# Performance work log

Measured on AMD Instinct MI355X. Metric: run time of the kernel, lower is better.

The kernel has to match this reference:

```python
import jax, jax.numpy as jnp
import numpy as np

N_NODES = 100000
N_EDGES = 1600000
IN_FEATS = 256
N_HIDDEN = 128
N_CLASSES = 40


def setup_inputs() -> dict:
    key = jax.random.key(0)
    k1, k2, k3, k4, k5 = jax.random.split(key, 5)
    features = jax.random.normal(k1, (N_NODES, IN_FEATS), dtype=jnp.float32)
    edge_src = jax.random.randint(k2, (N_EDGES,), 0, N_NODES, dtype=jnp.int64)
    edge_dst = jax.random.randint(k3, (N_EDGES,), 0, N_NODES, dtype=jnp.int64)
    # GraphConv weights (Glorot-ish scaling)
    W1 = jax.random.normal(k4, (IN_FEATS, N_HIDDEN), dtype=jnp.float32) / np.sqrt(IN_FEATS)
    b1 = jnp.zeros((N_HIDDEN,), dtype=jnp.float32)
    W2 = jax.random.normal(k5, (N_HIDDEN, N_CLASSES), dtype=jnp.float32) / np.sqrt(N_HIDDEN)
    b2 = jnpspace = None
    b2 = jnp.zeros((N_CLASSES,), dtype=jnp.float32)
    return {"features": features, "edge_src": edge_src, "edge_dst": edge_dst,
            "W1": W1, "b1": b1, "W2": W2, "b2": b2}


def _degree_norms(edge_src, edge_dst, n_nodes):
    ones = jnp.ones(edge_src.shape[0], dtype=jnp.float32)
    deg_out = jax.ops.segment_sum(ones, edge_src, num_segments=n_nodes)
    deg_in = jax.ops.segment_sum(ones, edge_dst, num_segments=n_nodes)
    norm_src = jax.lax.rsqrt(jnp.clip(deg_out, 1.0))  # D_out^{-1/2}
    norm_dst = jax.lax.rsqrt(jnp.clip(deg_in, 1.0))   # D_in^{-1/2}
    return norm_src, norm_dst


def _graph_conv(x, W, b, edge_src, edge_dst, norm_src, norm_dst, activation=None):
    # DGL GraphConv norm='both': out = D_in^{-1/2} A D_out^{-1/2} (x W) + b
    h = (x @ W) * norm_src[:, None]                       # transform then src-normalize
    agg = jax.ops.segment_sum(h[edge_src], edge_dst,
                              num_segments=x.shape[0])    # sparse neighbor aggregation
    out = agg * norm_dst[:, None] + b
    if activation is not None:
        out = activation(out)
    return out


def reference(features, edge_src, edge_dst, W1, b1, W2, b2):
    norm_src, norm_dst = _degree_norms(edge_src, edge_dst, features.shape[0])
    h = _graph_conv(features, W1, b1, edge_src, edge_dst, norm_src, norm_dst,
                    activation=jax.nn.relu)
    # dropout is identity in eval-mode reference
    out = _graph_conv(h, W2, b2, edge_src, edge_dst, norm_src, norm_dst)
    return out
```

## Files before the change

kernel.cpp:

```cpp
#include <hip/hip_runtime.h>
#include <hip/hip_bf16.h>
#include <hip/hip_fp16.h>

#define NN 100000
#define NE 1600000
#define KF 256
#define NH 128
#define NC 40
#define PAD 64
#define CMAX 63

#define NBLK_P 512
#define PCHUNK (NE / NBLK_P)
#define BUK 256
#define NBUK ((NN + BUK - 1) / BUK)
#define CAP 6144

typedef __attribute__((ext_vector_type(8))) short bf16x8;
typedef __attribute__((ext_vector_type(4))) float f32x4;


__device__ __forceinline__ float ldf(const void* p, size_t i, bool bf){
  return bf ? __bfloat162float(((const __hip_bfloat16*)p)[i]) : ((const float*)p)[i];
}
__device__ __forceinline__ void cv2(unsigned int v, float* o){
  union { unsigned int i; float f; } a, b;
  a.i = v << 16; b.i = v & 0xffff0000u;
  o[0] = a.f; o[1] = b.f;
}
__device__ __forceinline__ void splitbf(float f, short* h, short* lo){
  union { float f; unsigned int u; } a; a.f = f;
  *h = (short)(a.u >> 16);
  union { unsigned int u; float f; } c; c.u = a.u & 0xffff0000u;
  union { float f; unsigned int u; } d; d.f = f - c.f;
  *lo = (short)(d.u >> 16);
}

__global__ void k_sniff_edges(const unsigned int* __restrict__ e, unsigned int* __restrict__ flags){
  __shared__ unsigned int sh[256];
  unsigned int v = 0;
  for (int i = blockIdx.x * 256 + threadIdx.x; i < NE / 2; i += gridDim.x * 256)
    v |= e[2 * i + 1];
  sh[threadIdx.x] = v;
  __syncthreads();
  for (int off = 128; off; off >>= 1){
    if (threadIdx.x < off) sh[threadIdx.x] |= sh[threadIdx.x + off];
    __syncthreads();
  }
  if (threadIdx.x == 0 && sh[0]) atomicOr(&flags[0], sh[0]);
}

__global__ void k_sniff_float(const unsigned int* __restrict__ w, unsigned int* __restrict__ flags){
  __shared__ unsigned int sh[256];
  unsigned int hits = 0;
  for (int i = blockIdx.x * 256 + threadIdx.x; i < (1 << 20); i += gridDim.x * 256){
    unsigned int b = (w[i] >> 7) & 0xFFu;
    hits += (b >= 118u && b <= 130u) ? 1u : 0u;
  }
  sh[threadIdx.x] = hits;
  __syncthreads();
  for (int off = 128; off; off >>= 1){
    if (threadIdx.x < off) sh[threadIdx.x] += sh[threadIdx.x + off];
    __syncthreads();
  }
  if (threadIdx.x == 0) atomicAdd(&flags[1], sh[0]);
}

__device__ __forceinline__ int edge_at(const void* p, int e, bool is64){
  return is64 ? (int)((const long long*)p)[e] : ((const int*)p)[e];
}
__device__ __forceinline__ bool f_isbf(const unsigned int* flags){ return flags[1] > (1u << 19); }

__global__ __launch_bounds__(256) void k_part(const void* __restrict__ src,
    const void* __restrict__ dst, const unsigned int* __restrict__ flags,
    int* __restrict__ deg_out, int* __restrict__ gcur, unsigned int* __restrict__ part){
  __shared__ int cnt[NBUK];
  __shared__ int base[NBUK];
  const bool is64 = (flags[0] == 0u);
  const int beg = blockIdx.x * PCHUNK;
  const int end = min(beg + PCHUNK, NE);
  for (int t = threadIdx.x; t < NBUK; t += 256) cnt[t] = 0;
  __syncthreads();
  for (int e = beg + threadIdx.x; e < end; e += 256){
    int d = edge_at(dst, e, is64);
    atomicAdd(&cnt[d >> 8], 1);
  }
  __syncthreads();
  for (int t = threadIdx.x; t < NBUK; t += 256){
    int c = cnt[t];
    base[t] = c ? atomicAdd(&gcur[t], c) : 0;
    cnt[t] = 0;
  }
  __syncthreads();
  for (int e = beg + threadIdx.x; e < end; e += 256){
    int d = edge_at(dst, e, is64);
    int s = edge_at(src, e, is64);
    atomicAdd(&deg_out[s], 1);
    int b = d >> 8;
    int pos = base[b] + atomicAdd(&cnt[b], 1);
    if (pos < CAP)
      part[(size_t)b * CAP + pos] = ((unsigned int)s << 8) | (unsigned int)(d & 255);
  }
}

__global__ __launch_bounds__(256) void k_csr(const unsigned int* __restrict__ part,
    const int* __restrict__ gcur, int* __restrict__ fill, int* __restrict__ csr_pad){
  __shared__ int rows[256 * CMAX];
  __shared__ int fl[256];
  const int b = blockIdx.x;
  fl[threadIdx.x] = 0;
  __syncthreads();
  const int n = min(gcur[b], CAP);
  for (int i = threadIdx.x; i < n; i += 256){
    unsigned int e = part[(size_t)b * CAP + i];
    int r = (int)(e & 255u);
    int s = (int)(e >> 8);
    int pos = atomicAdd(&fl[r], 1);
    if (pos < CMAX) rows[r * CMAX + pos] = s;
  }
  __syncthreads();
  const int node0 = b * BUK;
  if (node0 + threadIdx.x < NN) fill[node0 + threadIdx.x] = fl[threadIdx.x];
  for (int idx = threadIdx.x; idx < 256 * CMAX; idx += 256){
    int r = idx / CMAX;
    int c = idx - r * CMAX;
    int node = node0 + r;
    if (node < NN) csr_pad[node * PAD + c] = rows[idx];
  }
}

__global__ void k_norms(const int* __restrict__ deg_out, const int* __restrict__ fill,
                        float* __restrict__ nsrc, float* __restrict__ ndst){
  int i = blockIdx.x * 256 + threadIdx.x;
  if (i < NN){
    nsrc[i] = rsqrtf(fmaxf((float)deg_out[i], 1.f));
    ndst[i] = rsqrtf(fmaxf((float)fill[i], 1.f));
  }
}

__global__ void k_w1s(const void* __restrict__ W1, const unsigned int* __restrict__ flags,
                      bf16x8* __restrict__ w1s){
  if (!f_isbf(flags)) return;
  int idx = blockIdx.x * 256 + threadIdx.x;
  if (idx >= 4096) return;
  int l    = idx & 63;
  int tile = idx >> 6;
  int kt   = tile >> 3;
  int nt   = tile & 7;
  int krow = kt * 32 + (l >> 4) * 8;
  int col  = nt * 16 + (l & 15);
  const unsigned short* w = (const unsigned short*)W1;
  bf16x8 v;
  #pragma unroll
  for (int j = 0; j < 8; j++)
    v[j] = (short)w[(size_t)(krow + j) * NH + col];
  w1s[idx] = v;
}
__global__ void k_w1s_f32(const void* __restrict__ W1, const unsigned int* __restrict__ flags,
                          bf16x8* __restrict__ w1h, bf16x8* __restrict__ w1l){
  if (f_isbf(flags)) return;
  int idx = blockIdx.x * 256 + threadIdx.x;
  if (idx >= 4096) return;
  int l    = idx & 63;
  int tile = idx >> 6;
  int kt   = tile >> 3;
  int nt   = tile & 7;
  int krow = kt * 32 + (l >> 4) * 8;
  int col  = nt * 16 + (l & 15);
  const float* w = (const float*)W1;
  bf16x8 vh, vl;
  #pragma unroll
  for (int j = 0; j < 8; j++){
    short h, lo;
    splitbf(w[(size_t)(krow + j) * NH + col], &h, &lo);
    vh[j] = h; vl[j] = lo;
  }
  w1h[idx] = vh;
  w1l[idx] = vl;
}

__global__ __launch_bounds__(256) void k_gemm1_mfma(const void* __restrict__ feat,
    const bf16x8* __restrict__ w1s, const unsigned int* __restrict__ flags,
    const float* __restrict__ nsrc, __half* __restrict__ h1){
  if (!f_isbf(flags)) return;
  const int t  = threadIdx.x;
  const int wv = t >> 6;
  const int l  = t & 63;
  const int row0 = blockIdx.x * 64 + wv * 16;
  const int arow = row0 + (l & 15);
  const short* fp = (const short*)feat;
  const size_t abase = (size_t)min(arow, NN - 1) * KF + (l >> 4) * 8;

  f32x4 acc[8];
  #pragma unroll
  for (int n = 0; n < 8; n++) acc[n] = (f32x4){0.f, 0.f, 0.f, 0.f};

  #pragma unroll 2
  for (int kt = 0; kt < 8; kt++){
    bf16x8 a = *(const bf16x8*)(fp + abase + kt * 32);
    #pragma unroll
    for (int n = 0; n < 8; n++){
      bf16x8 b = w1s[(kt * 8 + n) * 64 + l];
      acc[n] = __builtin_amdgcn_mfma_f32_16x16x32_bf16(a, b, acc[n], 0, 0, 0);
    }
  }
  const int rbase = row0 + (l >> 4) * 4;
  const int col   = l & 15;
  #pragma unroll
  for (int i = 0; i < 4; i++){
    int r = rbase + i;
    if (r < NN){
      float s = nsrc[r];
      #pragma unroll
      for (int n = 0; n < 8; n++)
        h1[(size_t)r * NH + n * 16 + col] = __float2half_rn(acc[n][i] * s);
    }
  }
}

__global__ __launch_bounds__(256) void k_gemm1_mf32(const float* __restrict__ feat,
    const bf16x8* __restrict__ w1h, const bf16x8* __restrict__ w1l,
    const unsigned int* __restrict__ flags,
    const float* __restrict__ nsrc, __half* __restrict__ h1){
  if (f_isbf(flags)) return;
  const int t  = threadIdx.x;
  const int wv = t >> 6;
  const int l  = t & 63;
  const int row0 = blockIdx.x * 128 + wv * 32;
  const int ar0 = row0 + (l & 15);
  const int ar1 = ar0 + 16;
  const float* fp0 = feat + (size_t)min(ar0, NN - 1) * KF + (l >> 4) * 8;
  const float* fp1 = feat + (size_t)min(ar1, NN - 1) * KF + (l >> 4) * 8;

  f32x4 acc[2][8];
  #pragma unroll
  for (int g = 0; g < 2; g++)
    #pragma unroll
    for (int n = 0; n < 8; n++) acc[g][n] = (f32x4){0.f, 0.f, 0.f, 0.f};

  for (int kt = 0; kt < 8; kt++){
    float4 u0 = *(const float4*)(fp0 + kt * 32);
    float4 u1 = *(const float4*)(fp0 + kt * 32 + 4);
    float4 v0 = *(const float4*)(fp1 + kt * 32);
    float4 v1 = *(const float4*)(fp1 + kt * 32 + 4);
    bf16x8 a0h, a0l, a1h, a1l;
    {
      const float* uf = (const float*)&u0;
      const float* vf = (const float*)&v0;
      #pragma unroll
      for (int j = 0; j < 4; j++){
        short h, lo;
        splitbf(uf[j], &h, &lo); a0h[j] = h; a0l[j] = lo;
        splitbf(vf[j], &h, &lo); a1h[j] = h; a1l[j] = lo;
      }
      const float* uf2 = (const float*)&u1;
      const float* vf2 = (const float*)&v1;
      #pragma unroll
      for (int j = 0; j < 4; j++){
        short h, lo;
        splitbf(uf2[j], &h, &lo); a0h[4 + j] = h; a0l[4 + j] = lo;
        splitbf(vf2[j], &h, &lo); a1h[4 + j] = h; a1l[4 + j] = lo;
      }
    }
    #pragma unroll
    for (int n = 0; n < 8; n++){
      bf16x8 bh = w1h[(kt * 8 + n) * 64 + l];
      bf16x8 bl = w1l[(kt * 8 + n) * 64 + l];
      acc[0][n] = __builtin_amdgcn_mfma_f32_16x16x32_bf16(a0h, bh, acc[0][n], 0, 0, 0);
      acc[0][n] = __builtin_amdgcn_mfma_f32_16x16x32_bf16(a0l, bh, acc[0][n], 0, 0, 0);
      acc[0][n] = __builtin_amdgcn_mfma_f32_16x16x32_bf16(a0h, bl, acc[0][n], 0, 0, 0);
      acc[1][n] = __builtin_amdgcn_mfma_f32_16x16x32_bf16(a1h, bh, acc[1][n], 0, 0, 0);
      acc[1][n] = __builtin_amdgcn_mfma_f32_16x16x32_bf16(a1l, bh, acc[1][n], 0, 0, 0);
      acc[1][n] = __builtin_amdgcn_mfma_f32_16x16x32_bf16(a1h, bl, acc[1][n], 0, 0, 0);
    }
  }
  const int col = l & 15;
  #pragma unroll
  for (int g = 0; g < 2; g++){
    const int rbase = row0 + g * 16 + (l >> 4) * 4;
    #pragma unroll
    for (int i = 0; i < 4; i++){
      int r = rbase + i;
      if (r < NN){
        float s = nsrc[r];
        #pragma unroll
        for (int n = 0; n < 8; n++)
          h1[(size_t)r * NH + n * 16 + col] = __float2half_rn(acc[g][n][i] * s);
      }
    }
  }
}

__global__ __launch_bounds__(256) void k_agg1(const int* __restrict__ csr_pad,
    const int* __restrict__ fill, const float* __restrict__ ndst,
    const unsigned int* __restrict__ h1w, const void* __restrict__ b1,
    const unsigned int* __restrict__ flags, float* __restrict__ x1){
  const bool isbf = f_isbf(flags);
  int node = blockIdx.x * 4 + (threadIdx.x >> 6);
  if (node >= NN) return;
  int lane = threadIdx.x & 63;
  int beg = node * PAD;
  int end = beg + min(fill[node], CMAX);
  float ax0 = 0.f, ay0 = 0.f, ax1 = 0.f, ay1 = 0.f;
  int e = beg;
  for (; e + 2 <= end; e += 2){
    int s0 = csr_pad[e], s1 = csr_pad[e+1];
    unsigned int u0 = h1w[(size_t)s0 * (NH/2) + lane];
    unsigned int u1 = h1w[(size_t)s1 * (NH/2) + lane];
    float2 v0 = __half22float2(*(__half2*)&u0);
    float2 v1 = __half22float2(*(__half2*)&u1);
    ax0 += v0.x; ay0 += v0.y;
    ax1 += v1.x; ay1 += v1.y;
  }
  if (e < end){
    int s0 = csr_pad[e];
    unsigned int u0 = h1w[(size_t)s0 * (NH/2) + lane];
    float2 v0 = __half22float2(*(__half2*)&u0);
    ax0 += v0.x; ay0 += v0.y;
  }
  float nd = ndst[node];
  float bx = ldf(b1, lane*2,   isbf);
  float by = ldf(b1, lane*2+1, isbf);
  float2 o;
  o.x = fmaxf((ax0 + ax1) * nd + bx, 0.f);
  o.y = fmaxf((ay0 + ay1) * nd + by, 0.f);
  ((float2*)(x1 + (size_t)node * NH))[lane] = o;
}

__global__ __launch_bounds__(256) void k_gemm2(const float* __restrict__ x1,
    const void* __restrict__ W2, const unsigned int* __restrict__ flags,
    const float* __restrict__ nsrc, __half* __restrict__ h2){
  const bool isbf = f_isbf(flags);
  __shared__ float Xs[128][68];
  __shared__ float Ws[64][44];
  const int t = threadIdx.x;
  const int row0 = blockIdx.x * 128;
  const int cg = t & 7;
  const int rg = t >> 3;
  float acc[4][5];
  #pragma unroll
  for (int i = 0; i < 4; i++)
    #pragma unroll
    for (int j = 0; j < 5; j++) acc[i][j] = 0.f;

  for (int kc = 0; kc < NH; kc += 64){
    #pragma unroll
    for (int q0 = 0; q0 < 8; q0++){
      int q  = t + q0 * 256;
      int r  = q >> 4;
      int kq = (q & 15) * 4;
      int grow = row0 + r;
      float4 v;
      if (grow < NN) v = *(const float4*)(x1 + (size_t)grow * NH + kc + kq);
      else { v.x = v.y = v.z = v.w = 0.f; }
      *(float4*)&Xs[r][kq] = v;
    }
    #pragma unroll
    for (int q0 = 0; q0 < 10; q0++){
      int idx = t + q0 * 256;
      int k = idx / 40;
      int c = idx - k * 40;
      Ws[k][c] = ldf(W2, (size_t)(kc + k) * NC + c, isbf);
    }
    __syncthreads();
    #pragma unroll 4
    for (int k = 0; k < 64; k++){
      float a0 = Xs[rg*4+0][k];
      float a1 = Xs[rg*4+1][k];
      float a2 = Xs[rg*4+2][k];
      float a3 = Xs[rg*4+3][k];
      float b[5];
      #pragma unroll
      for (int j = 0; j < 5; j++) b[j] = Ws[k][cg*5 + j];
      #pragma unroll
      for (int j = 0; j < 5; j++){
        acc[0][j] += a0 * b[j];
        acc[1][j] += a1 * b[j];
        acc[2][j] += a2 * b[j];
        acc[3][j] += a3 * b[j];
      }
    }
    __syncthreads();
  }
  #pragma unroll
  for (int i = 0; i < 4; i++){
    int r = row0 + rg*4 + i;
    if (r < NN){
      float s = nsrc[r];
      #pragma unroll
      for (int j = 0; j < 5; j++)
        h2[(size_t)r * NC + cg*5 + j] = __float2half_rn(acc[i][j] * s);
    }
  }
}

__global__ __launch_bounds__(256) void k_agg2(const int* __restrict__ csr_pad,
    const int* __restrict__ fill, const float* __restrict__ ndst,
    const unsigned int* __restrict__ h2w, const void* __restrict__ b2,
    const unsigned int* __restrict__ flags, float* __restrict__ out){
  const bool isbf = f_isbf(flags);
  int node = blockIdx.x * 4 + (threadIdx.x >> 6);
  if (node >= NN) return;
  int lane = threadIdx.x & 63;
  int beg = node * PAD;
  int end = beg + min(fill[node], CMAX);
  if (lane < NC/2){
    float ax0 = 0.f, ay0 = 0.f, ax1 = 0.f, ay1 = 0.f;
    int e = beg;
    for (; e + 2 <= end; e += 2){
      int s0 = csr_pad[e], s1 = csr_pad[e+1];
      unsigned int u0 = h2w[(size_t)s0 * (NC/2) + lane];
      unsigned int u1 = h2w[(size_t)s1 * (NC/2) + lane];
      float2 v0 = __half22float2(*(__half2*)&u0);
      float2 v1 = __half22float2(*(__half2*)&u1);
      ax0 += v0.x; ay0 += v0.y;
      ax1 += v1.x; ay1 += v1.y;
    }
    if (e < end){
      int s0 = csr_pad[e];
      unsigned int u0 = h2w[(size_t)s0 * (NC/2) + lane];
      float2 v0 = __half22float2(*(__half2*)&u0);
      ax0 += v0.x; ay0 += v0.y;
    }
    float nd = ndst[node];
    float2 o;
    o.x = (ax0 + ax1) * nd + ldf(b2, 2*lane,   isbf);
    o.y = (ay0 + ay1) * nd + ldf(b2, 2*lane+1, isbf);
    ((float2*)(out + (size_t)node * NC))[lane] = o;
  }
}

extern "C" void kernel_launch(void* const* d_in, const int* in_sizes, int n_in,
                              void* d_out, int out_size, void* d_ws, size_t ws_size,
                              hipStream_t stream) {
  const long long SZ_FEAT = (long long)NN * KF, SZ_E = NE, SZ_W1 = (long long)KF * NH,
                  SZ_B1 = NH, SZ_W2 = (long long)NH * NC, SZ_B2 = NC;
  int i_feat = -1, i_e1 = -1, i_e2 = -1, i_W1 = -1, i_b1 = -1, i_W2 = -1, i_b2 = -1;
  auto m = [](long long s, long long z){ return s == z || s == 4*z || s == 8*z || s == 2*z; };
  for (int i = 0; i < n_in; i++){
    long long s = in_sizes[i];
    if      (m(s, SZ_FEAT)) i_feat = i;
    else if (m(s, SZ_E))    { if (i_e1 < 0) i_e1 = i; else i_e2 = i; }
    else if (m(s, SZ_W1))   i_W1 = i;
    else if (m(s, SZ_B1))   i_b1 = i;
    else if (m(s, SZ_W2))   i_W2 = i;
    else if (m(s, SZ_B2))   i_b2 = i;
  }
  if (i_feat < 0 || i_e2 < 0 || i_W1 < 0 || i_b1 < 0 || i_W2 < 0 || i_b2 < 0){
    i_feat = 0; i_e1 = 1; i_e2 = 2; i_W1 = 3; i_b1 = 4; i_W2 = 5; i_b2 = 6;
  }
  const void* feat = d_in[i_feat];
  const void* esrc = d_in[i_e1];
  const void* edst = d_in[i_e2];
  const void* W1   = d_in[i_W1];
  const void* b1   = d_in[i_b1];
  const void* W2   = d_in[i_W2];
  const void* b2   = d_in[i_b2];
  float* out = (float*)d_out;

  int* deg_out        = (int*)d_ws;
  int* fill           = deg_out + NN;
  unsigned int* flags = (unsigned int*)(fill + NN);
  int* gcur           = (int*)(flags + 4);
  float* norm_src     = (float*)(gcur + 400);
  float* norm_dst     = norm_src + NN;
  int* csr_pad        = (int*)(norm_dst + NN);
  __half* h1          = (__half*)(csr_pad + (size_t)NN * PAD);
  float* x1           = (float*)(h1 + (size_t)NN * NH);
  __half* h2          = h1;
  unsigned int* part  = (unsigned int*)x1;
  bf16x8* w1h         = (bf16x8*)((char*)x1 + (16u << 20));
  bf16x8* w1l         = w1h + 4096;

  hipMemsetAsync(deg_out, 0, ((size_t)2 * NN + 4 + 400) * sizeof(int), stream);

  k_sniff_edges<<<400, 256, 0, stream>>>((const unsigned int*)esrc, flags);
  k_sniff_float<<<256, 256, 0, stream>>>((const unsigned int*)feat, flags);
  k_w1s    <<<16, 256, 0, stream>>>(W1, flags, w1h);
  k_w1s_f32<<<16, 256, 0, stream>>>(W1, flags, w1h, w1l);
  k_part<<<NBLK_P, 256, 0, stream>>>(esrc, edst, flags, deg_out, gcur, part);
  k_csr <<<NBUK,   256, 0, stream>>>(part, gcur, fill, csr_pad);
  k_norms<<<(NN + 255) / 256, 256, 0, stream>>>(deg_out, fill, norm_src, norm_dst);

  k_gemm1_mfma<<<(NN + 63) / 64,   256, 0, stream>>>(feat, w1h, flags, norm_src, h1);
  k_gemm1_mf32<<<(NN + 127) / 128, 256, 0, stream>>>((const float*)feat, w1h, w1l,
                                                     flags, norm_src, h1);
  k_agg1 <<<(NN + 3) / 4, 256, 0, stream>>>(csr_pad, fill, norm_dst,
                                            (const unsigned int*)h1, b1, flags, x1);
  k_gemm2<<<(NN + 127) / 128, 256, 0, stream>>>(x1, W2, flags, norm_src, h2);
  k_agg2 <<<(NN + 3) / 4, 256, 0, stream>>>(csr_pad, fill, norm_dst,
                                            (const unsigned int*)h2, b2, flags, out);
}
```

Baseline: 568.9 us.

## Store h1 in column-chunked layout and split layer-1 aggregation by feature group

GEMM1 now writes h1 as eight column chunks of 16 features, each stored contiguously over all nodes. The layer-1 aggregation is split so each block handles one 16-feature chunk for 32 nodes, with 8 lanes per node. The aim is to shrink the working set of each gather pass so random neighbour reads hit L2 more often. In exchange, each node's CSR row is read eight times and the gathers become narrow 32-byte accesses. The unused bf16 GEMM1 path and its weight-swizzle kernel are also removed, so bf16 feature inputs no longer have a matching path.

```diff
diff --git a/kernel.cpp b/kernel.cpp
--- a/kernel.cpp
+++ b/kernel.cpp
@@ -22,11 +22,6 @@
 
 __device__ __forceinline__ float ldf(const void* p, size_t i, bool bf){
   return bf ? __bfloat162float(((const __hip_bfloat16*)p)[i]) : ((const float*)p)[i];
-}
-__device__ __forceinline__ void cv2(unsigned int v, float* o){
-  union { unsigned int i; float f; } a, b;
-  a.i = v << 16; b.i = v & 0xffff0000u;
-  o[0] = a.f; o[1] = b.f;
 }
 __device__ __forceinline__ void splitbf(float f, short* h, short* lo){
   union { float f; unsigned int u; } a; a.f = f;
@@ -138,24 +133,6 @@
   }
 }
 
-__global__ void k_w1s(const void* __restrict__ W1, const unsigned int* __restrict__ flags,
-                      bf16x8* __restrict__ w1s){
-  if (!f_isbf(flags)) return;
-  int idx = blockIdx.x * 256 + threadIdx.x;
-  if (idx >= 4096) return;
-  int l    = idx & 63;
-  int tile = idx >> 6;
-  int kt   = tile >> 3;
-  int nt   = tile & 7;
-  int krow = kt * 32 + (l >> 4) * 8;
-  int col  = nt * 16 + (l & 15);
-  const unsigned short* w = (const unsigned short*)W1;
-  bf16x8 v;
-  #pragma unroll
-  for (int j = 0; j < 8; j++)
-    v[j] = (short)w[(size_t)(krow + j) * NH + col];
-  w1s[idx] = v;
-}
 __global__ void k_w1s_f32(const void* __restrict__ W1, const unsigned int* __restrict__ flags,
                           bf16x8* __restrict__ w1h, bf16x8* __restrict__ w1l){
   if (f_isbf(flags)) return;
@@ -177,45 +154,6 @@
   }
   w1h[idx] = vh;
   w1l[idx] = vl;
-}
-
-__global__ __launch_bounds__(256) void k_gemm1_mfma(const void* __restrict__ feat,
-    const bf16x8* __restrict__ w1s, const unsigned int* __restrict__ flags,
-    const float* __restrict__ nsrc, __half* __restrict__ h1){
-  if (!f_isbf(flags)) return;
-  const int t  = threadIdx.x;
-  const int wv = t >> 6;
-  const int l  = t & 63;
-  const int row0 = blockIdx.x * 64 + wv * 16;
-  const int arow = row0 + (l & 15);
-  const short* fp = (const short*)feat;
-  const size_t abase = (size_t)min(arow, NN - 1) * KF + (l >> 4) * 8;
-
-  f32x4 acc[8];
-  #pragma unroll
-  for (int n = 0; n < 8; n++) acc[n] = (f32x4){0.f, 0.f, 0.f, 0.f};
-
-  #pragma unroll 2
-  for (int kt = 0; kt < 8; kt++){
-    bf16x8 a = *(const bf16x8*)(fp + abase + kt * 32);
-    #pragma unroll
-    for (int n = 0; n < 8; n++){
-      bf16x8 b = w1s[(kt * 8 + n) * 64 + l];
-      acc[n] = __builtin_amdgcn_mfma_f32_16x16x32_bf16(a, b, acc[n], 0, 0, 0);
-    }
-  }
-  const int rbase = row0 + (l >> 4) * 4;
-  const int col   = l & 15;
-  #pragma unroll
-  for (int i = 0; i < 4; i++){
-    int r = rbase + i;
-    if (r < NN){
-      float s = nsrc[r];
-      #pragma unroll
-      for (int n = 0; n < 8; n++)
-        h1[(size_t)r * NH + n * 16 + col] = __float2half_rn(acc[n][i] * s);
-    }
-  }
 }
 
 __global__ __launch_bounds__(256) void k_gemm1_mf32(const float* __restrict__ feat,
@@ -285,28 +223,29 @@
         float s = nsrc[r];
         #pragma unroll
         for (int n = 0; n < 8; n++)
-          h1[(size_t)r * NH + n * 16 + col] = __float2half_rn(acc[g][n][i] * s);
+          h1[((size_t)n * NN + r) * 16 + col] = __float2half_rn(acc[g][n][i] * s);
       }
     }
   }
 }
 
-__global__ __launch_bounds__(256) void k_agg1(const int* __restrict__ csr_pad,
+__global__ __launch_bounds__(256) void k_agg1c(const int* __restrict__ csr_pad,
     const int* __restrict__ fill, const float* __restrict__ ndst,
-    const unsigned int* __restrict__ h1w, const void* __restrict__ b1,
+    const unsigned int* __restrict__ h1c, const void* __restrict__ b1,
     const unsigned int* __restrict__ flags, float* __restrict__ x1){
   const bool isbf = f_isbf(flags);
-  int node = blockIdx.x * 4 + (threadIdx.x >> 6);
-  if (node >= NN) return;
-  int lane = threadIdx.x & 63;
-  int beg = node * PAD;
-  int end = beg + min(fill[node], CMAX);
+  const int g    = blockIdx.x & 7;
+  const int node = (blockIdx.x >> 3) * 32 + (threadIdx.x >> 3);
+  const int lane = threadIdx.x & 7;
+  const unsigned int* hb = h1c + (size_t)g * NN * 8;
+  const int beg = node * PAD;
+  const int end = beg + min(fill[node], CMAX);
   float ax0 = 0.f, ay0 = 0.f, ax1 = 0.f, ay1 = 0.f;
   int e = beg;
   for (; e + 2 <= end; e += 2){
-    int s0 = csr_pad[e], s1 = csr_pad[e+1];
-    unsigned int u0 = h1w[(size_t)s0 * (NH/2) + lane];
-    unsigned int u1 = h1w[(size_t)s1 * (NH/2) + lane];
+    int s0 = csr_pad[e], s1 = csr_pad[e + 1];
+    unsigned int u0 = hb[(size_t)s0 * 8 + lane];
+    unsigned int u1 = hb[(size_t)s1 * 8 + lane];
     float2 v0 = __half22float2(*(__half2*)&u0);
     float2 v1 = __half22float2(*(__half2*)&u1);
     ax0 += v0.x; ay0 += v0.y;
@@ -314,17 +253,18 @@
   }
   if (e < end){
     int s0 = csr_pad[e];
-    unsigned int u0 = h1w[(size_t)s0 * (NH/2) + lane];
+    unsigned int u0 = hb[(size_t)s0 * 8 + lane];
     float2 v0 = __half22float2(*(__half2*)&u0);
     ax0 += v0.x; ay0 += v0.y;
   }
   float nd = ndst[node];
-  float bx = ldf(b1, lane*2,   isbf);
-  float by = ldf(b1, lane*2+1, isbf);
+  int f0 = g * 16 + lane * 2;
+  float bx = ldf(b1, f0,     isbf);
+  float by = ldf(b1, f0 + 1, isbf);
   float2 o;
   o.x = fmaxf((ax0 + ax1) * nd + bx, 0.f);
   o.y = fmaxf((ay0 + ay1) * nd + by, 0.f);
-  ((float2*)(x1 + (size_t)node * NH))[lane] = o;
+  ((float2*)(x1 + (size_t)node * NH))[g * 8 + lane] = o;
 }
 
 __global__ __launch_bounds__(256) void k_gemm2(const float* __restrict__ x1,
@@ -476,17 +416,15 @@
 
   k_sniff_edges<<<400, 256, 0, stream>>>((const unsigned int*)esrc, flags);
   k_sniff_float<<<256, 256, 0, stream>>>((const unsigned int*)feat, flags);
-  k_w1s    <<<16, 256, 0, stream>>>(W1, flags, w1h);
   k_w1s_f32<<<16, 256, 0, stream>>>(W1, flags, w1h, w1l);
   k_part<<<NBLK_P, 256, 0, stream>>>(esrc, edst, flags, deg_out, gcur, part);
   k_csr <<<NBUK,   256, 0, stream>>>(part, gcur, fill, csr_pad);
   k_norms<<<(NN + 255) / 256, 256, 0, stream>>>(deg_out, fill, norm_src, norm_dst);
 
-  k_gemm1_mfma<<<(NN + 63) / 64,   256, 0, stream>>>(feat, w1h, flags, norm_src, h1);
   k_gemm1_mf32<<<(NN + 127) / 128, 256, 0, stream>>>((const float*)feat, w1h, w1l,
                                                      flags, norm_src, h1);
-  k_agg1 <<<(NN + 3) / 4, 256, 0, stream>>>(csr_pad, fill, norm_dst,
-                                            (const unsigned int*)h1, b1, flags, x1);
+  k_agg1c<<<(NN / 32) * 8, 256, 0, stream>>>(csr_pad, fill, norm_dst,
+                                             (const unsigned int*)h1, b1, flags, x1);
   k_gemm2<<<(NN + 127) / 128, 256, 0, stream>>>(x1, W2, flags, norm_src, h2);
   k_agg2 <<<(NN + 3) / 4, 256, 0, stream>>>(csr_pad, fill, norm_dst,
                                             (const unsigned int*)h2, b2, flags, out);
```

Result: slower. 605.9 us (+6.5%).
